# Optimization experiments

Measured on AMD Instinct MI355X. Metric: run time of the kernel, lower is better.

Reference implementation:

```python
import jax, jax.numpy as jnp
import numpy as np

SEQ_LEN = 48
OUT_DIM = 3
EMB_DIM = 32
HID_DIM = 96
BATCH = 131072


def setup_inputs() -> dict:
    key = jax.random.key(0)
    ks = jax.random.split(key, 12)
    s_emb = 1.0 / np.sqrt(OUT_DIM)
    s_gru = 1.0 / np.sqrt(HID_DIM)
    s_out = 1.0 / np.sqrt(HID_DIM)
    u = lambda k, shp, s: jax.random.uniform(k, shp, jnp.float32, -s, s)
    return {
        "last_pos_rel": jax.random.normal(ks[0], (BATCH, OUT_DIM), jnp.float32),
        "past_encoded": jax.random.normal(ks[1], (1, BATCH, HID_DIM // 2), jnp.float32),
        "future_encoded": jax.random.normal(ks[2], (1, BATCH, HID_DIM // 2), jnp.float32),
        "W_emb": u(ks[3], (EMB_DIM, OUT_DIM), s_emb),
        "b_emb": u(ks[4], (EMB_DIM,), s_emb),
        "W_ih": u(ks[5], (3 * HID_DIM, EMB_DIM), s_gru),
        "W_hh": u(ks[6], (3 * HID_DIM, HID_DIM), s_gru),
        "b_ih": u(ks[7], (3 * HID_DIM,), s_gru),
        "b_hh": u(ks[8], (3 * HID_DIM,), s_gru),
        "W_out": u(ks[9], (OUT_DIM, HID_DIM), s_out),
        "b_out": u(ks[10], (OUT_DIM,), s_out),
    }


def reference(last_pos_rel, past_encoded, future_encoded, W_emb, b_emb,
              W_ih, W_hh, b_ih, b_hh, W_out, b_out):
    # initial hidden state: concat of the two 48-dim encodings -> (B, 96)
    h0 = jnp.concatenate([past_encoded, future_encoded], axis=2)[0]
    # initial decoder input: spatial embedding of last relative position
    x0 = last_pos_rel @ W_emb.T + b_emb  # (B, EMB)

    def step(carry, _):
        h, x = carry
        gx = x @ W_ih.T + b_ih   # (B, 3H)
        gh = h @ W_hh.T + b_hh   # (B, 3H)
        gxr, gxz, gxn = jnp.split(gx, 3, axis=-1)
        ghr, ghz, ghn = jnp.split(gh, 3, axis=-1)
        r = jax.nn.sigmoid(gxr + ghr)
        z = jax.nn.sigmoid(gxz + ghz)
        n = jnp.tanh(gxn + r * ghn)
        h_new = (1.0 - z) * n + z * h
        rel_pos = h_new @ W_out.T + b_out       # (B, 3)
        x_new = rel_pos @ W_emb.T + b_emb       # (B, EMB)
        return (h_new, x_new), rel_pos

    _, pred_traj = jax.lax.scan(step, (h0, x0), None, length=SEQ_LEN)
    return pred_traj  # (SEQ_LEN, B, 3)
```

## Files before the change

kernel.cpp:

```cpp
#include <hip/hip_runtime.h>
#include <hip/hip_bf16.h>
#include <type_traits>

#define SEQ_LEN 48
#define HID     96
#define NB      131072
#define MROWS   304
#define ABYTES  (MROWS*HID*2)
#define COEF_OFF_F (ABYTES/4)
#define COEF_FLOATS (96*16)
#define BOUT_OFF_F (COEF_OFF_F + COEF_FLOATS)
#define LDS_U4  ((ABYTES + COEF_FLOATS*4)/16)

typedef __attribute__((ext_vector_type(4))) float f32x4;
typedef __attribute__((ext_vector_type(8))) __bf16 bf16x8;
typedef unsigned int uint;
typedef unsigned short ushort;

__device__ __forceinline__ float sigm2(float xp) {
    return __builtin_amdgcn_rcpf(1.f + __builtin_amdgcn_exp2f(-xp));
}
__device__ __forceinline__ float tanh2(float yp) {
    return 1.f - 2.f * __builtin_amdgcn_rcpf(__builtin_amdgcn_exp2f(yp) + 1.f);
}
__device__ __forceinline__ uint packbf(float a, float b) {
    ushort lo = __builtin_bit_cast(ushort, __float2bfloat16(a));
    ushort hi = __builtin_bit_cast(ushort, __float2bfloat16(b));
    return (uint)lo | ((uint)hi << 16);
}

__global__ void fold_k(const float* __restrict__ W_emb, const float* __restrict__ b_emb,
                       const float* __restrict__ W_ih,  const float* __restrict__ W_hh,
                       const float* __restrict__ b_ih,  const float* __restrict__ b_hh,
                       const float* __restrict__ W_out, const float* __restrict__ b_out,
                       void* wsv)
{
    const float L2E  = 1.44269504088896340736f;
    const float L2E2 = 2.f * L2E;
    ushort* A  = (ushort*)wsv;
    float*  CF = (float*)wsv + COEF_OFF_F;
    float*  BO = (float*)wsv + BOUT_OFF_F;
    int g = blockIdx.x * 64 + threadIdx.x;
    if (g < 3) BO[g] = b_out[g];

    auto wxe_row = [&](int gg, float* w, float& bx) {
        w[0] = w[1] = w[2] = 0.f; bx = b_ih[gg];
        for (int e = 0; e < 32; e++) {
            float wi = W_ih[gg * 32 + e];
            w[0] += wi * W_emb[e * 3 + 0];
            w[1] += wi * W_emb[e * 3 + 1];
            w[2] += wi * W_emb[e * 3 + 2];
            bx   += wi * b_emb[e];
        }
    };

    if (g < MROWS) {
        float w[3] = {0.f, 0.f, 0.f}, bx = 0.f;
        if (g < 192) wxe_row(g, w, bx);
        for (int k = 0; k < HID; k++) {
            float val;
            if      (g < 192) val = (W_hh[g * HID + k] + w[0]*W_out[0*HID+k] + w[1]*W_out[1*HID+k] + w[2]*W_out[2*HID+k]) * L2E;
            else if (g < 288) val = W_hh[g * HID + k] * L2E2;
            else if (g < 291) val = W_out[(g - 288) * HID + k];
            else              val = 0.f;
            int t = g >> 4, c = k >> 5, l = (g & 15) | (((k >> 3) & 3) << 4), i = k & 7;
            A[((t * 3 + c) * 64 + l) * 8 + i] = __builtin_bit_cast(ushort, __float2bfloat16(val));
        }
    }
    if (g < 96) {
        int j = g;
        float wn[3], bxn; wxe_row(192 + j, wn, bxn);
        float wr[3], bxr; wxe_row(j,        wr, bxr);
        float wz[3], bxz; wxe_row(96 + j,   wz, bxz);
        float quads[4][4] = {
            { wn[0]*L2E2, wn[1]*L2E2, wn[2]*L2E2, bxn*L2E2 },
            { b_hh[192 + j]*L2E2,
              (bxr + b_hh[j]      + wr[0]*b_out[0] + wr[1]*b_out[1] + wr[2]*b_out[2]) * L2E,
              (bxz + b_hh[96 + j] + wz[0]*b_out[0] + wz[1]*b_out[1] + wz[2]*b_out[2]) * L2E,
              0.f },
            { wr[0]*L2E, wr[1]*L2E, wr[2]*L2E, wz[0]*L2E },
            { wz[1]*L2E, wz[2]*L2E, 0.f, 0.f }
        };
        int qj = (j >> 2) & 3;
        float* row = CF + j * 16;
        for (int L = 0; L < 4; ++L) {
            int p = (L + qj) & 3;
            row[p * 4 + 0] = quads[L][0];
            row[p * 4 + 1] = quads[L][1];
            row[p * 4 + 2] = quads[L][2];
            row[p * 4 + 3] = quads[L][3];
        }
    }
}

__global__ __launch_bounds__(512, 4)
void gru_mfma(const float* __restrict__ last_pos, const float* __restrict__ past,
              const float* __restrict__ fut, const void* __restrict__ wsv,
              float* __restrict__ out)
{
    __shared__ uint4 sb[LDS_U4];
    const int tid = threadIdx.x;
    const uint4* gsrc = (const uint4*)wsv;
    #pragma unroll
    for (int it = 0; it < 8; ++it) { int idx = tid + it * 512; if (idx < LDS_U4) sb[idx] = gsrc[idx]; }
    __syncthreads();

    const float* CF  = (const float*)sb + COEF_OFF_F;
    const float* BOg = (const float*)wsv + BOUT_OFF_F;
    const float bo[3] = {BOg[0], BOg[1], BOg[2]};

    const int lane = tid & 63;
    const int wid  = tid >> 6;
    const int b    = lane & 15;
    const int q    = lane >> 4;
    const int row0 = blockIdx.x * 128 + wid * 16 + b;

    uint hpk[6][2];
    #pragma unroll
    for (int t = 0; t < 6; ++t) {
        const float* src = (t < 3) ? (past + (size_t)row0 * 48 + t * 16 + q * 4)
                                   : (fut  + (size_t)row0 * 48 + (t - 3) * 16 + q * 4);
        f32x4 v = *(const f32x4*)src;
        hpk[t][0] = packbf(v[0], v[1]);
        hpk[t][1] = packbf(v[2], v[3]);
    }

    const int idxA = 4 * (b | ((((q << 1) + 0) & 3) << 4));
    const int idxB = 4 * (b | ((((q << 1) + 1) & 3) << 4));
    uint4 bfu[3];
    auto do_exchange = [&]() {
        #pragma unroll
        for (int c = 0; c < 3; ++c)
            #pragma unroll
            for (int dd = 0; dd < 4; ++dd) {
                int idx = (dd < 2) ? idxA : idxB;
                int va = __builtin_amdgcn_ds_bpermute(idx, (int)hpk[2 * c][dd & 1]);
                int vb = __builtin_amdgcn_ds_bpermute(idx, (int)hpk[2 * c + 1][dd & 1]);
                bfu[c][dd] = (uint)((lane < 32) ? va : vb);
            }
    };
    do_exchange();

    float pc[3];
    pc[0] = last_pos[(size_t)row0 * 3 + 0];
    pc[1] = last_pos[(size_t)row0 * 3 + 1];
    pc[2] = last_pos[(size_t)row0 * 3 + 2];

    const f32x4 zero4 = {0.f, 0.f, 0.f, 0.f};
    const int p0r = (0 + q) & 3, p1r = (1 + q) & 3, p2r = (2 + q) & 3, p3r = (3 + q) & 3;

    auto tile18 = [&]() -> f32x4 {
        f32x4 a18;
        #pragma unroll
        for (int c = 0; c < 3; ++c) {
            bf16x8 a = __builtin_bit_cast(bf16x8, sb[(18 * 3 + c) * 64 + lane]);
            bf16x8 bb = __builtin_bit_cast(bf16x8, bfu[c]);
            a18 = __builtin_amdgcn_mfma_f32_16x16x32_bf16(a, bb, (c == 0) ? zero4 : a18, 0, 0, 0);
        }
        return a18;
    };

    auto do_groups = [&](auto FIRST_c, const float* d0) {
        constexpr bool FIRST = decltype(FIRST_c)::value;
        #pragma unroll
        for (int t = 0; t < 6; ++t) {
            f32x4 aR, aZ, aN;
            #pragma unroll
            for (int c = 0; c < 3; ++c) {
                bf16x8 fr = __builtin_bit_cast(bf16x8, sb[((t)      * 3 + c) * 64 + lane]);
                bf16x8 fz = __builtin_bit_cast(bf16x8, sb[((6 + t)  * 3 + c) * 64 + lane]);
                bf16x8 fn = __builtin_bit_cast(bf16x8, sb[((12 + t) * 3 + c) * 64 + lane]);
                bf16x8 bb = __builtin_bit_cast(bf16x8, bfu[c]);
                aR = __builtin_amdgcn_mfma_f32_16x16x32_bf16(fr, bb, (c == 0) ? zero4 : aR, 0, 0, 0);
                aZ = __builtin_amdgcn_mfma_f32_16x16x32_bf16(fz, bb, (c == 0) ? zero4 : aZ, 0, 0, 0);
                aN = __builtin_amdgcn_mfma_f32_16x16x32_bf16(fn, bb, (c == 0) ? zero4 : aN, 0, 0, 0);
            }
            const float* cbase = CF + (16 * t + 4 * q) * 16;
            uint np0 = 0, np1 = 0;
            #pragma unroll
            for (int r = 0; r < 4; ++r) {
                f32x4 ca = *(const f32x4*)(cbase + 16 * r + 4 * p0r);
                f32x4 cb = *(const f32x4*)(cbase + 16 * r + 4 * p1r);
                float sr  = aR[r] + cb[1];
                float sz  = aZ[r] + cb[2];
                float ghn = aN[r] + cb[0];
                float gxn = ca[3] + pc[0]*ca[0] + pc[1]*ca[1] + pc[2]*ca[2];
                if constexpr (FIRST) {
                    f32x4 c2 = *(const f32x4*)(cbase + 16 * r + 4 * p2r);
                    f32x4 c3 = *(const f32x4*)(cbase + 16 * r + 4 * p3r);
                    sr += d0[0]*c2[0] + d0[1]*c2[1] + d0[2]*c2[2];
                    sz += d0[0]*c2[3] + d0[1]*c3[0] + d0[2]*c3[1];
                }
                float rg = sigm2(sr);
                float zg = sigm2(sz);
                float ng = tanh2(gxn + rg * ghn);
                uint pk = hpk[t][r >> 1];
                float hold = __builtin_bit_cast(float, (r & 1) ? (pk & 0xffff0000u) : (pk << 16));
                float hv = ng + zg * (hold - ng);
                ushort hb = __builtin_bit_cast(ushort, __float2bfloat16(hv));
                if      (r == 0) np0 = hb;
                else if (r == 1) np0 |= (uint)hb << 16;
                else if (r == 2) np1 = hb;
                else             np1 |= (uint)hb << 16;
            }
            hpk[t][0] = np0;
            hpk[t][1] = np1;
            __builtin_amdgcn_sched_barrier(0);
        }
    };

    {
        f32x4 a18 = tile18();
        float d0[3];
        #pragma unroll
        for (int o = 0; o < 3; ++o) {
            float po = a18[o] + bo[o];
            float pb = __builtin_bit_cast(float,
                        __builtin_amdgcn_ds_bpermute(4 * b, __builtin_bit_cast(int, po)));
            d0[o] = pc[o] - pb;
        }
        __builtin_amdgcn_sched_barrier(0);
        do_groups(std::integral_constant<bool, true>{}, d0);
        do_exchange();
    }

    #pragma unroll 1
    for (int s = 1; s < SEQ_LEN; ++s) {
        f32x4 a18 = tile18();
        #pragma unroll
        for (int o = 0; o < 3; ++o) {
            float po = a18[o] + bo[o];
            float pb = __builtin_bit_cast(float,
                        __builtin_amdgcn_ds_bpermute(4 * b, __builtin_bit_cast(int, po)));
            if (q == 0) out[((size_t)(s - 1) * NB + row0) * 3 + o] = po;
            pc[o] = pb;
        }
        __builtin_amdgcn_sched_barrier(0);
        do_groups(std::integral_constant<bool, false>{}, nullptr);
        do_exchange();
    }

    {
        f32x4 f18 = tile18();
        if (q == 0) {
            #pragma unroll
            for (int o = 0; o < 3; ++o)
                out[((size_t)47 * NB + row0) * 3 + o] = f18[o] + bo[o];
        }
    }
}

extern "C" void kernel_launch(void* const* d_in, const int* in_sizes, int n_in,
                              void* d_out, int out_size, void* d_ws, size_t ws_size,
                              hipStream_t stream)
{
    const float* last_pos = (const float*)d_in[0];
    const float* past     = (const float*)d_in[1];
    const float* fut      = (const float*)d_in[2];
    const float* W_emb    = (const float*)d_in[3];
    const float* b_emb    = (const float*)d_in[4];
    const float* W_ih     = (const float*)d_in[5];
    const float* W_hh     = (const float*)d_in[6];
    const float* b_ih     = (const float*)d_in[7];
    const float* b_hh     = (const float*)d_in[8];
    const float* W_out    = (const float*)d_in[9];
    const float* b_out    = (const float*)d_in[10];
    float* out = (float*)d_out;

    hipLaunchKernelGGL(fold_k, dim3(5), dim3(64), 0, stream,
                       W_emb, b_emb, W_ih, W_hh, b_ih, b_hh, W_out, b_out, d_ws);
    hipLaunchKernelGGL(gru_mfma, dim3(NB / 128), dim3(512), 0, stream,
                       last_pos, past, fut, d_ws, out);
}
```

Before: 871.2 us.

## Fold n-gate input projection into an extra MFMA on hidden state

The n-gate input contribution (W_ih_n·W_emb·W_out) is precomputed as a bf16 matrix, so gxn now comes from a fourth MFMA per tile instead of scalar FMAs on the previous output. This removes the per-step ds_bpermute broadcast of predicted positions and the associated FMA work. Bias coefficients now live in global memory rather than LDS. The cost is an extra MFMA per group, with its weights fetched from global memory (GX) on every step instead of LDS, plus more global coefficient reads and lower precision from bf16 rounding of the folded weights.

```diff
diff --git a/kernel.cpp b/kernel.cpp
--- a/kernel.cpp
+++ b/kernel.cpp
@@ -7,10 +7,11 @@
 #define NB      131072
 #define MROWS   304
 #define ABYTES  (MROWS*HID*2)
-#define COEF_OFF_F (ABYTES/4)
-#define COEF_FLOATS (96*16)
-#define BOUT_OFF_F (COEF_OFF_F + COEF_FLOATS)
-#define LDS_U4  ((ABYTES + COEF_FLOATS*4)/16)
+#define A_U4    (ABYTES/16)
+#define GX_OFF_U4 3648
+#define CB_OFF_F  19200
+#define PE_OFF_F  19584
+#define BO_OFF_F  20736
 
 typedef __attribute__((ext_vector_type(4))) float f32x4;
 typedef __attribute__((ext_vector_type(8))) __bf16 bf16x8;
@@ -37,9 +38,11 @@
 {
     const float L2E  = 1.44269504088896340736f;
     const float L2E2 = 2.f * L2E;
-    ushort* A  = (ushort*)wsv;
-    float*  CF = (float*)wsv + COEF_OFF_F;
-    float*  BO = (float*)wsv + BOUT_OFF_F;
+    ushort* A   = (ushort*)wsv;
+    ushort* GXu = (ushort*)wsv + ABYTES/2;
+    float*  CB  = (float*)wsv + CB_OFF_F;
+    float*  PE  = (float*)wsv + PE_OFF_F;
+    float*  BO  = (float*)wsv + BO_OFF_F;
     int g = blockIdx.x * 64 + threadIdx.x;
     if (g < 3) BO[g] = b_out[g];
 
@@ -72,24 +75,18 @@
         float wn[3], bxn; wxe_row(192 + j, wn, bxn);
         float wr[3], bxr; wxe_row(j,        wr, bxr);
         float wz[3], bxz; wxe_row(96 + j,   wz, bxz);
-        float quads[4][4] = {
-            { wn[0]*L2E2, wn[1]*L2E2, wn[2]*L2E2, bxn*L2E2 },
-            { b_hh[192 + j]*L2E2,
-              (bxr + b_hh[j]      + wr[0]*b_out[0] + wr[1]*b_out[1] + wr[2]*b_out[2]) * L2E,
-              (bxz + b_hh[96 + j] + wz[0]*b_out[0] + wz[1]*b_out[1] + wz[2]*b_out[2]) * L2E,
-              0.f },
-            { wr[0]*L2E, wr[1]*L2E, wr[2]*L2E, wz[0]*L2E },
-            { wz[1]*L2E, wz[2]*L2E, 0.f, 0.f }
-        };
-        int qj = (j >> 2) & 3;
-        float* row = CF + j * 16;
-        for (int L = 0; L < 4; ++L) {
-            int p = (L + qj) & 3;
-            row[p * 4 + 0] = quads[L][0];
-            row[p * 4 + 1] = quads[L][1];
-            row[p * 4 + 2] = quads[L][2];
-            row[p * 4 + 3] = quads[L][3];
-        }
+        for (int k = 0; k < HID; k++) {
+            float v = L2E2 * (wn[0]*W_out[0*HID+k] + wn[1]*W_out[1*HID+k] + wn[2]*W_out[2*HID+k]);
+            int t2 = j >> 4, c = k >> 5, l = (j & 15) | (((k >> 3) & 3) << 4), i = k & 7;
+            GXu[((t2 * 3 + c) * 64 + l) * 8 + i] = __builtin_bit_cast(ushort, __float2bfloat16(v));
+        }
+        CB[j*4 + 0] = b_hh[192 + j] * L2E2;
+        CB[j*4 + 1] = (bxr + b_hh[j]      + wr[0]*b_out[0] + wr[1]*b_out[1] + wr[2]*b_out[2]) * L2E;
+        CB[j*4 + 2] = (bxz + b_hh[96 + j] + wz[0]*b_out[0] + wz[1]*b_out[1] + wz[2]*b_out[2]) * L2E;
+        CB[j*4 + 3] = (bxn + wn[0]*b_out[0] + wn[1]*b_out[1] + wn[2]*b_out[2]) * L2E2;
+        PE[j*12 + 0] = wr[0]*L2E;  PE[j*12 + 1] = wr[1]*L2E;  PE[j*12 + 2] = wr[2]*L2E;  PE[j*12 + 3] = wz[0]*L2E;
+        PE[j*12 + 4] = wz[1]*L2E;  PE[j*12 + 5] = wz[2]*L2E;  PE[j*12 + 6] = wn[0]*L2E2; PE[j*12 + 7] = wn[1]*L2E2;
+        PE[j*12 + 8] = wn[2]*L2E2; PE[j*12 + 9] = 0.f;        PE[j*12 +10] = 0.f;        PE[j*12 +11] = 0.f;
     }
 }
 
@@ -98,15 +95,17 @@
               const float* __restrict__ fut, const void* __restrict__ wsv,
               float* __restrict__ out)
 {
-    __shared__ uint4 sb[LDS_U4];
+    __shared__ uint4 sb[A_U4];
     const int tid = threadIdx.x;
     const uint4* gsrc = (const uint4*)wsv;
     #pragma unroll
-    for (int it = 0; it < 8; ++it) { int idx = tid + it * 512; if (idx < LDS_U4) sb[idx] = gsrc[idx]; }
+    for (int it = 0; it < 8; ++it) { int idx = tid + it * 512; if (idx < A_U4) sb[idx] = gsrc[idx]; }
     __syncthreads();
 
-    const float* CF  = (const float*)sb + COEF_OFF_F;
-    const float* BOg = (const float*)wsv + BOUT_OFF_F;
+    const uint4* GX  = gsrc + GX_OFF_U4;
+    const float* CBg = (const float*)wsv + CB_OFF_F;
+    const float* PEg = (const float*)wsv + PE_OFF_F;
+    const float* BOg = (const float*)wsv + BO_OFF_F;
     const float bo[3] = {BOg[0], BOg[1], BOg[2]};
 
     const int lane = tid & 63;
@@ -141,13 +140,7 @@
     };
     do_exchange();
 
-    float pc[3];
-    pc[0] = last_pos[(size_t)row0 * 3 + 0];
-    pc[1] = last_pos[(size_t)row0 * 3 + 1];
-    pc[2] = last_pos[(size_t)row0 * 3 + 2];
-
     const f32x4 zero4 = {0.f, 0.f, 0.f, 0.f};
-    const int p0r = (0 + q) & 3, p1r = (1 + q) & 3, p2r = (2 + q) & 3, p3r = (3 + q) & 3;
 
     auto tile18 = [&]() -> f32x4 {
         f32x4 a18;
@@ -164,32 +157,35 @@
         constexpr bool FIRST = decltype(FIRST_c)::value;
         #pragma unroll
         for (int t = 0; t < 6; ++t) {
-            f32x4 aR, aZ, aN;
+            f32x4 aR, aZ, aN, aX;
             #pragma unroll
             for (int c = 0; c < 3; ++c) {
                 bf16x8 fr = __builtin_bit_cast(bf16x8, sb[((t)      * 3 + c) * 64 + lane]);
                 bf16x8 fz = __builtin_bit_cast(bf16x8, sb[((6 + t)  * 3 + c) * 64 + lane]);
                 bf16x8 fn = __builtin_bit_cast(bf16x8, sb[((12 + t) * 3 + c) * 64 + lane]);
+                bf16x8 fx = __builtin_bit_cast(bf16x8, GX[(t * 3 + c) * 64 + lane]);
                 bf16x8 bb = __builtin_bit_cast(bf16x8, bfu[c]);
                 aR = __builtin_amdgcn_mfma_f32_16x16x32_bf16(fr, bb, (c == 0) ? zero4 : aR, 0, 0, 0);
                 aZ = __builtin_amdgcn_mfma_f32_16x16x32_bf16(fz, bb, (c == 0) ? zero4 : aZ, 0, 0, 0);
                 aN = __builtin_amdgcn_mfma_f32_16x16x32_bf16(fn, bb, (c == 0) ? zero4 : aN, 0, 0, 0);
+                aX = __builtin_amdgcn_mfma_f32_16x16x32_bf16(fx, bb, (c == 0) ? zero4 : aX, 0, 0, 0);
             }
-            const float* cbase = CF + (16 * t + 4 * q) * 16;
             uint np0 = 0, np1 = 0;
             #pragma unroll
             for (int r = 0; r < 4; ++r) {
-                f32x4 ca = *(const f32x4*)(cbase + 16 * r + 4 * p0r);
-                f32x4 cb = *(const f32x4*)(cbase + 16 * r + 4 * p1r);
-                float sr  = aR[r] + cb[1];
-                float sz  = aZ[r] + cb[2];
-                float ghn = aN[r] + cb[0];
-                float gxn = ca[3] + pc[0]*ca[0] + pc[1]*ca[1] + pc[2]*ca[2];
+                int j = 16 * t + 4 * q + r;
+                f32x4 cbq = *(const f32x4*)(CBg + j * 4);
+                float sr  = aR[r] + cbq[1];
+                float sz  = aZ[r] + cbq[2];
+                float ghn = aN[r] + cbq[0];
+                float gxn = aX[r] + cbq[3];
                 if constexpr (FIRST) {
-                    f32x4 c2 = *(const f32x4*)(cbase + 16 * r + 4 * p2r);
-                    f32x4 c3 = *(const f32x4*)(cbase + 16 * r + 4 * p3r);
-                    sr += d0[0]*c2[0] + d0[1]*c2[1] + d0[2]*c2[2];
-                    sz += d0[0]*c2[3] + d0[1]*c3[0] + d0[2]*c3[1];
+                    f32x4 pe0 = *(const f32x4*)(PEg + j * 12);
+                    f32x4 pe1 = *(const f32x4*)(PEg + j * 12 + 4);
+                    f32x4 pe2 = *(const f32x4*)(PEg + j * 12 + 8);
+                    sr  += d0[0]*pe0[0] + d0[1]*pe0[1] + d0[2]*pe0[2];
+                    sz  += d0[0]*pe0[3] + d0[1]*pe1[0] + d0[2]*pe1[1];
+                    gxn += d0[0]*pe1[2] + d0[1]*pe1[3] + d0[2]*pe2[0];
                 }
                 float rg = sigm2(sr);
                 float zg = sigm2(sz);
@@ -210,6 +206,10 @@
     };
 
     {
+        float pc[3];
+        pc[0] = last_pos[(size_t)row0 * 3 + 0];
+        pc[1] = last_pos[(size_t)row0 * 3 + 1];
+        pc[2] = last_pos[(size_t)row0 * 3 + 2];
         f32x4 a18 = tile18();
         float d0[3];
         #pragma unroll
@@ -227,13 +227,10 @@
     #pragma unroll 1
     for (int s = 1; s < SEQ_LEN; ++s) {
         f32x4 a18 = tile18();
-        #pragma unroll
-        for (int o = 0; o < 3; ++o) {
-            float po = a18[o] + bo[o];
-            float pb = __builtin_bit_cast(float,
-                        __builtin_amdgcn_ds_bpermute(4 * b, __builtin_bit_cast(int, po)));
-            if (q == 0) out[((size_t)(s - 1) * NB + row0) * 3 + o] = po;
-            pc[o] = pb;
+        if (q == 0) {
+            #pragma unroll
+            for (int o = 0; o < 3; ++o)
+                out[((size_t)(s - 1) * NB + row0) * 3 + o] = a18[o] + bo[o];
         }
         __builtin_amdgcn_sched_barrier(0);
         do_groups(std::integral_constant<bool, false>{}, nullptr);
```

Result: slower. 1.923 ms (+120.8%).
